# Kernel optimization log

Hardware: AMD Instinct MI355X
Metric: run time of the kernel (lower is better)

## Reference

```python
import jax, jax.numpy as jnp
import numpy as np

B, N, C = 8, 1374, 768
H = 12
HD = C // H  # 64
HIDDEN = int(C * 4.0)  # 3072
EPS = 1e-5


def setup_inputs() -> dict:
    key = jax.random.key(0)
    ks = jax.random.split(key, 12)
    s = 0.02
    return {
        "x": jax.random.normal(ks[0], (B, N, C), jnp.float32),
        "rope_freqs": jax.random.normal(ks[1], (1, N, 1, HD), jnp.float32),
        "ln1_g": jnp.ones((C,), jnp.float32),
        "ln1_b": jnp.zeros((C,), jnp.float32),
        "qkv_w": jax.random.normal(ks[2], (3 * C, C), jnp.float32) * s,
        "qkv_b": jnp.zeros((3 * C,), jnp.float32),
        "proj_w": jax.random.normal(ks[3], (C, C), jnp.float32) * s,
        "proj_b": jnp.zeros((C,), jnp.float32),
        "ln2_g": jnp.ones((C,), jnp.float32),
        "ln2_b": jnp.zeros((C,), jnp.float32),
        "w1": jax.random.normal(ks[4], (HIDDEN, C), jnp.float32) * s,
        "b1": jnp.zeros((HIDDEN,), jnp.float32),
        "w2": jax.random.normal(ks[5], (HIDDEN, C), jnp.float32) * s,
        "b2": jnp.zeros((HIDDEN,), jnp.float32),
        "w3": jax.random.normal(ks[6], (C, HIDDEN), jnp.float32) * s,
        "b3": jnp.zeros((C,), jnp.float32),
    }


def _layernorm(x, g, b):
    mu = jnp.mean(x, axis=-1, keepdims=True)
    var = jnp.mean(jnp.square(x - mu), axis=-1, keepdims=True)
    return (x - mu) * jax.lax.rsqrt(var + EPS) * g + b


def _rotate_half(x):
    x1, x2 = jnp.split(x, 2, axis=-1)
    return jnp.concatenate([-x2, x1], axis=-1)


def _apply_rope(q, k, freqs):
    # freqs: [1, N, 1, HD] -> [1, 1, N, HD] (matches torch permute(0,2,1,3))
    f = jnp.transpose(freqs, (0, 2, 1, 3))
    cos, sin = jnp.cos(f), jnp.sin(f)
    q_rot = q * cos + _rotate_half(q) * sin
    k_rot = k * cos + _rotate_half(k) * sin
    return q_rot, k_rot


def reference(x, rope_freqs, ln1_g, ln1_b, qkv_w, qkv_b, proj_w, proj_b,
              ln2_g, ln2_b, w1, b1, w2, b2, w3, b3):
    scale = HD ** -0.5
    # --- Attention branch ---
    h = _layernorm(x, ln1_g, ln1_b)
    qkv = jnp.einsum('bnc,dc->bnd', h, qkv_w) + qkv_b          # [B,N,3C]
    qkv = qkv.reshape(B, N, 3, H, HD).transpose(2, 0, 3, 1, 4)  # [3,B,H,N,HD]
    q, k, v = qkv[0], qkv[1], qkv[2]
    # rope_freqs covers all N tokens -> n_special = 0 path
    q, k = _apply_rope(q, k, rope_freqs)
    attn = jnp.einsum('bhnd,bhmd->bhnm', q, k) * scale          # [B,H,N,N]
    attn = jax.nn.softmax(attn, axis=-1)
    o = jnp.einsum('bhnm,bhmd->bhnd', attn, v)                  # [B,H,N,HD]
    o = o.transpose(0, 2, 1, 3).reshape(B, N, C)
    o = jnp.einsum('bnc,dc->bnd', o, proj_w) + proj_b
    x = x + o
    # --- SwiGLU MLP branch ---
    h2 = _layernorm(x, ln2_g, ln2_b)
    x1 = jnp.einsum('bnc,hc->bnh', h2, w1) + b1
    x2 = jnp.einsum('bnc,hc->bnh', h2, w2) + b2
    hid = jax.nn.silu(x1) * x2
    mlp_out = jnp.einsum('bnh,ch->bnc', hid, w3) + b3
    return x + mlp_out
```

## Files before the change

### kernel.cpp

```cpp
#include <hip/hip_runtime.h>
#include <stdint.h>

#define B_ 8
#define N_ 1374
#define C_ 768
#define H_ 12
#define HD_ 64
#define HID_ 3072
#define M_ (B_*N_)
#define MPAD_ 11008
#define QT_ 22
#define QT2_ 11

typedef __attribute__((ext_vector_type(8))) short short8;
typedef __attribute__((ext_vector_type(4))) float f32x4;
typedef __attribute__((ext_vector_type(4))) _Float16 half4;
typedef __attribute__((ext_vector_type(2))) _Float16 half2v;

__device__ __forceinline__ unsigned short f2bf(float f) {
  unsigned u = __float_as_uint(f);
  u += 0x7FFF + ((u >> 16) & 1);
  return (unsigned short)(u >> 16);
}
__device__ __forceinline__ float bf2f(unsigned short h) {
  return __uint_as_float(((unsigned)h) << 16);
}

__device__ __forceinline__ half2v pkrtz(float a, float b) {
  return __builtin_bit_cast(half2v, __builtin_amdgcn_cvt_pkrtz(a, b));
}

#if __has_builtin(__builtin_amdgcn_global_load_lds)
#define HAVE_GLL 1
#endif

__device__ __forceinline__ void gld16(const unsigned short* g, unsigned short* l) {
#ifdef HAVE_GLL
  __builtin_amdgcn_global_load_lds((const __attribute__((address_space(1))) void*)g,
                                   (__attribute__((address_space(3))) void*)l, 16, 0, 0);
#else
  *(short8*)l = *(const short8*)g;
#endif
}

__global__ __launch_bounds__(256) void cvt5_kernel(
    const float* __restrict__ s0, const float* __restrict__ s1,
    const float* __restrict__ s2, const float* __restrict__ s3,
    const float* __restrict__ s4, unsigned short* __restrict__ out) {
  int id = blockIdx.x * 256 + threadIdx.x;
  const float* src; int off;
  if (id < 442368)        { src = s0; off = id; }
  else if (id < 589824)   { src = s1; off = id - 442368; }
  else if (id < 1179648)  { src = s2; off = id - 589824; }
  else if (id < 1769472)  { src = s3; off = id - 1179648; }
  else                    { src = s4; off = id - 1769472; }
  float4 v = ((const float4*)src)[off];
  ushort4 o;
  o.x = f2bf(v.x); o.y = f2bf(v.y); o.z = f2bf(v.z); o.w = f2bf(v.w);
  ((ushort4*)out)[id] = o;
}

__global__ __launch_bounds__(256) void ln_kernel(const float* __restrict__ in,
    const float* __restrict__ g, const float* __restrict__ bta,
    unsigned short* __restrict__ out) {
  int row = blockIdx.x;
  int t = threadIdx.x;
  const float* xr = in + (size_t)row * C_;
  float v0 = xr[t], v1 = xr[t + 256], v2 = xr[t + 512];
  float s1 = v0 + v1 + v2;
  float s2 = v0*v0 + v1*v1 + v2*v2;
  for (int off = 1; off < 64; off <<= 1) {
    s1 += __shfl_xor(s1, off, 64);
    s2 += __shfl_xor(s2, off, 64);
  }
  __shared__ float r1[4], r2[4];
  int wave = t >> 6, lane = t & 63;
  if (lane == 0) { r1[wave] = s1; r2[wave] = s2; }
  __syncthreads();
  float tot1 = r1[0] + r1[1] + r1[2] + r1[3];
  float tot2 = r2[0] + r2[1] + r2[2] + r2[3];
  float mu = tot1 * (1.0f / C_);
  float var = tot2 * (1.0f / C_) - mu * mu;
  float rs = rsqrtf(var + 1e-5f);
  size_t ob = (size_t)row * C_;
  out[ob + t]       = f2bf((v0 - mu) * rs * g[t]       + bta[t]);
  out[ob + t + 256] = f2bf((v1 - mu) * rs * g[t + 256] + bta[t + 256]);
  out[ob + t + 512] = f2bf((v2 - mu) * rs * g[t + 512] + bta[t + 512]);
}

template<int EPI, int ROPE, int TM, int SWZ>
__global__ __launch_bounds__(256, (TM == 64) ? 4 : 2) void gemm_bt(
    const unsigned short* __restrict__ A,
    const unsigned short* __restrict__ W,
    void* __restrict__ outp,
    const float* __restrict__ bias0,
    const float* __restrict__ resid,
    const float* __restrict__ freqs,
    int K, int ldo, int Mvalid, int X)
{
  constexpr int MI = TM / 32;
  __shared__ __align__(16) unsigned short As[2][TM * 32];
  __shared__ __align__(16) unsigned short Bs[2][4096];
  const int t = threadIdx.x;
  const int lane = t & 63;
  const int wave = t >> 6;
  const int wm = (wave >> 1) * (TM / 2);
  const int wn = (wave & 1) * 64;
  const int lr = lane & 15;
  const int lg = lane >> 4;
  const int lk = lg * 8;
  int bx, by;
  if (SWZ) {
    int Y = gridDim.x / X;
    int lin = blockIdx.x;
    int sgsz = X * 8;
    int sg = lin / sgsz;
    int base_y = sg * 8;
    int rows = Y - base_y; if (rows > 8) rows = 8;
    int within = lin - sg * sgsz;
    by = base_y + within % rows;
    bx = within / rows;
  } else {
    bx = blockIdx.x % X;
    by = blockIdx.x / X;
  }
  const int tm0 = by * TM;
  const int tn0 = bx * 128;
  const int r0 = t >> 2;
  const int c0 = (t & 3) * 8;
  const unsigned short* ga0 = A + (size_t)(tm0 + r0) * K + c0;
  const unsigned short* ga1 = A + (size_t)(tm0 + 64 + r0) * K + c0;
  const unsigned short* gb0 = W + (size_t)(tn0 + r0) * K + c0;
  const unsigned short* gb1 = W + (size_t)(tn0 + 64 + r0) * K + c0;
  f32x4 zero = {0.f, 0.f, 0.f, 0.f};
  f32x4 acc[MI][4];
#pragma unroll
  for (int mi = 0; mi < MI; ++mi)
#pragma unroll
    for (int ni = 0; ni < 4; ++ni) acc[mi][ni] = zero;

  for (int kt = 0; kt < K; kt += 64) {
    __syncthreads();
    gld16(ga0 + kt,      &As[0][t * 8]);
    gld16(ga0 + kt + 32, &As[1][t * 8]);
    if (TM == 128) {
      gld16(ga1 + kt,      &As[0][2048 + t * 8]);
      gld16(ga1 + kt + 32, &As[1][2048 + t * 8]);
    }
    gld16(gb0 + kt,      &Bs[0][t * 8]);
    gld16(gb1 + kt,      &Bs[0][2048 + t * 8]);
    gld16(gb0 + kt + 32, &Bs[1][t * 8]);
    gld16(gb1 + kt + 32, &Bs[1][2048 + t * 8]);
    __syncthreads();
#pragma unroll
    for (int u = 0; u < 2; ++u) {
      short8 af[MI], bfr[4];
#pragma unroll
      for (int mi = 0; mi < MI; ++mi) af[mi] = *(const short8*)&As[u][(wm + mi * 16 + lr) * 32 + lk];
#pragma unroll
      for (int ni = 0; ni < 4; ++ni) bfr[ni] = *(const short8*)&Bs[u][(wn + ni * 16 + lr) * 32 + lk];
#pragma unroll
      for (int mi = 0; mi < MI; ++mi)
#pragma unroll
        for (int ni = 0; ni < 4; ++ni)
          acc[mi][ni] = __builtin_amdgcn_mfma_f32_16x16x32_bf16(af[mi], bfr[ni], acc[mi][ni], 0, 0, 0);
    }
  }

  if (EPI == 0) {
    bool dorope = ROPE && ((tn0 + wn) < 1536);
#pragma unroll
    for (int mi = 0; mi < MI; ++mi) {
#pragma unroll
      for (int p = 0; p < 2; ++p) {
        int col1 = tn0 + wn + p * 16 + lr;
        int col2 = col1 + 32;
        float bv1 = bias0[col1], bv2 = bias0[col2];
        int e = p * 16 + lr;
#pragma unroll
        for (int r = 0; r < 4; ++r) {
          int row = tm0 + wm + mi * 16 + lg * 4 + r;
          float v1 = acc[mi][p][r] + bv1;
          float v2 = acc[mi][p + 2][r] + bv2;
          float o1 = v1, o2 = v2;
          if (dorope) {
            int n = row % N_;
            float f1 = freqs[n * HD_ + e];
            float f2 = freqs[n * HD_ + e + 32];
            float c1, s1, c2, s2;
            __sincosf(f1, &s1, &c1);
            __sincosf(f2, &s2, &c2);
            o1 = v1 * c1 - v2 * s1;
            o2 = v2 * c2 + v1 * s2;
          }
          size_t base = (size_t)row * ldo;
          ((unsigned short*)outp)[base + col1] = f2bf(o1);
          ((unsigned short*)outp)[base + col2] = f2bf(o2);
        }
      }
    }
  } else {
#pragma unroll
    for (int mi = 0; mi < MI; ++mi) {
#pragma unroll
      for (int ni = 0; ni < 4; ++ni) {
        int col = tn0 + wn + ni * 16 + lr;
        float bval = bias0[col];
#pragma unroll
        for (int r = 0; r < 4; ++r) {
          int row = tm0 + wm + mi * 16 + lg * 4 + r;
          float v = acc[mi][ni][r] + bval;
          size_t idx = (size_t)row * ldo + col;
          if (EPI == 1) {
            if (row < Mvalid) ((float*)outp)[idx] = resid[idx] + v;
          } else {
            if (row < Mvalid) ((float*)outp)[idx] = ((float*)outp)[idx] + v;
          }
        }
      }
    }
  }
}

__global__ __launch_bounds__(256, 2) void gemm_w12_swiglu(
    const unsigned short* __restrict__ A,
    const unsigned short* __restrict__ W1,
    const unsigned short* __restrict__ W2,
    unsigned short* __restrict__ hid,
    const float* __restrict__ b1,
    const float* __restrict__ b2)
{
  __shared__ __align__(16) unsigned short As[2][4096];
  __shared__ __align__(16) unsigned short B1s[2][2048];
  __shared__ __align__(16) unsigned short B2s[2][2048];
  const int t = threadIdx.x;
  const int lane = t & 63;
  const int wave = t >> 6;
  const int wm = (wave >> 1) * 64;
  const int wn = (wave & 1) * 32;
  const int lr = lane & 15;
  const int lg = lane >> 4;
  const int lk = lg * 8;
  const int tm0 = blockIdx.y * 128;
  const int tn0 = blockIdx.x * 64;
  const int r0 = t >> 2;
  const int c0 = (t & 3) * 8;
  const unsigned short* ga0 = A + (size_t)(tm0 + r0) * 768 + c0;
  const unsigned short* ga1 = A + (size_t)(tm0 + 64 + r0) * 768 + c0;
  const unsigned short* g1 = W1 + (size_t)(tn0 + r0) * 768 + c0;
  const unsigned short* g2 = W2 + (size_t)(tn0 + r0) * 768 + c0;
  f32x4 zero = {0.f, 0.f, 0.f, 0.f};
  f32x4 acc1[4][2], acc2[4][2];
#pragma unroll
  for (int mi = 0; mi < 4; ++mi)
#pragma unroll
    for (int ni = 0; ni < 2; ++ni) { acc1[mi][ni] = zero; acc2[mi][ni] = zero; }

  for (int kt = 0; kt < 768; kt += 64) {
    __syncthreads();
    gld16(ga0 + kt,      &As[0][t * 8]);
    gld16(ga1 + kt,      &As[0][2048 + t * 8]);
    gld16(ga0 + kt + 32, &As[1][t * 8]);
    gld16(ga1 + kt + 32, &As[1][2048 + t * 8]);
    gld16(g1 + kt,       &B1s[0][t * 8]);
    gld16(g1 + kt + 32,  &B1s[1][t * 8]);
    gld16(g2 + kt,       &B2s[0][t * 8]);
    gld16(g2 + kt + 32,  &B2s[1][t * 8]);
    __syncthreads();
#pragma unroll
    for (int u = 0; u < 2; ++u) {
      short8 af[4], b1f[2], b2f[2];
#pragma unroll
      for (int mi = 0; mi < 4; ++mi) af[mi] = *(const short8*)&As[u][(wm + mi * 16 + lr) * 32 + lk];
#pragma unroll
      for (int ni = 0; ni < 2; ++ni) {
        b1f[ni] = *(const short8*)&B1s[u][(wn + ni * 16 + lr) * 32 + lk];
        b2f[ni] = *(const short8*)&B2s[u][(wn + ni * 16 + lr) * 32 + lk];
      }
#pragma unroll
      for (int mi = 0; mi < 4; ++mi)
#pragma unroll
        for (int ni = 0; ni < 2; ++ni) {
          acc1[mi][ni] = __builtin_amdgcn_mfma_f32_16x16x32_bf16(af[mi], b1f[ni], acc1[mi][ni], 0, 0, 0);
          acc2[mi][ni] = __builtin_amdgcn_mfma_f32_16x16x32_bf16(af[mi], b2f[ni], acc2[mi][ni], 0, 0, 0);
        }
    }
  }
#pragma unroll
  for (int mi = 0; mi < 4; ++mi) {
#pragma unroll
    for (int ni = 0; ni < 2; ++ni) {
      int col = tn0 + wn + ni * 16 + lr;
      float bv1 = b1[col], bv2 = b2[col];
#pragma unroll
      for (int r = 0; r < 4; ++r) {
        int row = tm0 + wm + mi * 16 + lg * 4 + r;
        float a1 = acc1[mi][ni][r] + bv1;
        float a2 = acc2[mi][ni][r] + bv2;
        float h = a1 / (1.f + __expf(-a1)) * a2;
        hid[(size_t)row * HID_ + col] = f2bf(h);
      }
    }
  }
}

struct FalseT { static constexpr bool value = false; };
struct TrueT  { static constexpr bool value = true;  };

__global__ __launch_bounds__(256, 2) void attn_kernel(
    const unsigned short* __restrict__ qkv,
    unsigned short* __restrict__ o2)
{
  __shared__ __align__(16) unsigned short Ks[2][64 * 80];
  __shared__ __align__(16) _Float16 Vt[2][64 * 72];
  int bidx = blockIdx.x;
  int qt = bidx % QT2_;
  int bh = bidx / QT2_;
  int head = bh % H_;
  int b = bh / H_;
  int t = threadIdx.x, lane = t & 63, wave = t >> 6;
  int lr = lane & 15, lg = lane >> 4;

  short8 bq[2][2];
#pragma unroll
  for (int s = 0; s < 2; ++s) {
    int m = qt * 128 + wave * 32 + s * 16 + lr;
    int mc = (m < N_) ? m : (N_ - 1);
    const unsigned short* qrow = qkv + (size_t)(b * N_ + mc) * 2304 + head * HD_;
    bq[s][0] = *(const short8*)(qrow + lg * 8);
    bq[s][1] = *(const short8*)(qrow + 32 + lg * 8);
  }

  f32x4 zero = {0.f, 0.f, 0.f, 0.f};
  f32x4 acc[2][4];
#pragma unroll
  for (int s = 0; s < 2; ++s)
#pragma unroll
    for (int dt = 0; dt < 4; ++dt) acc[s][dt] = zero;
  float den[2] = {0.f, 0.f};

  const int kr0 = t >> 3;
  const int kc  = (t & 7) * 8;
  const int vp  = t & 31;
  const int vc  = t >> 5;
  const unsigned short* kbase = qkv + (size_t)(b * N_) * 2304 + 768  + head * HD_ + kc;
  const unsigned short* vbase = qkv + (size_t)(b * N_) * 2304 + 1536 + head * HD_ + vc * 8;

  short8 krg[2], vrg[2];
  auto issue = [&](int jt) {
    int j0 = jt * 64 + kr0;        if (j0 >= N_) j0 = N_ - 1;
    int j1 = jt * 64 + kr0 + 32;   if (j1 >= N_) j1 = N_ - 1;
    int vj0 = jt * 64 + 2 * vp;    if (vj0 >= N_) vj0 = N_ - 1;
    int vj1 = jt * 64 + 2 * vp + 1; if (vj1 >= N_) vj1 = N_ - 1;
    krg[0] = *(const short8*)(kbase + (size_t)j0 * 2304);
    krg[1] = *(const short8*)(kbase + (size_t)j1 * 2304);
    vrg[0] = *(const short8*)(vbase + (size_t)vj0 * 2304);
    vrg[1] = *(const short8*)(vbase + (size_t)vj1 * 2304);
  };

  auto compute = [&](int jt, const unsigned short* ksb, const _Float16* vtb, auto tailc) {
    constexpr bool TAIL = decltype(tailc)::value;
#pragma unroll
    for (int st = 0; st < 4; ++st) {
      short8 ak0 = *(const short8*)&ksb[(st * 16 + lr) * 80 + lg * 8];
      short8 ak1 = *(const short8*)&ksb[(st * 16 + lr) * 80 + 32 + lg * 8];
      int jb = jt * 64 + st * 16 + lg * 4;
      half4 pf[2];
#pragma unroll
      for (int s = 0; s < 2; ++s) {
        f32x4 sc = zero;
        sc = __builtin_amdgcn_mfma_f32_16x16x32_bf16(ak0, bq[s][0], sc, 0, 0, 0);
        sc = __builtin_amdgcn_mfma_f32_16x16x32_bf16(ak1, bq[s][1], sc, 0, 0, 0);
        float p[4];
#pragma unroll
        for (int r = 0; r < 4; ++r) {
          float pv = exp2f(sc[r] * 0.18033688011112f);
          if (TAIL) pv = (jb + r < N_) ? pv : 0.f;
          p[r] = pv;
        }
        den[s] += (p[0] + p[1]) + (p[2] + p[3]);
        union { half4 v; half2v h[2]; } pu;
        pu.h[0] = pkrtz(p[0], p[1]);
        pu.h[1] = pkrtz(p[2], p[3]);
        pf[s] = pu.v;
      }
#pragma unroll
      for (int dt = 0; dt < 4; ++dt) {
        half4 bv = *(const half4*)&vtb[(dt * 16 + lr) * 72 + st * 16 + lg * 4];
        acc[0][dt] = __builtin_amdgcn_mfma_f32_16x16x16f16(pf[0], bv, acc[0][dt], 0, 0, 0);
        acc[1][dt] = __builtin_amdgcn_mfma_f32_16x16x16f16(pf[1], bv, acc[1][dt], 0, 0, 0);
      }
    }
  };

  issue(0);
  int cur = 0;
  for (int jt = 0; jt < QT_; ++jt) {
    unsigned short* ksb = &Ks[cur][0];
    _Float16* vtb = &Vt[cur][0];
    *(short8*)&ksb[kr0 * 80 + kc] = krg[0];
    *(short8*)&ksb[(kr0 + 32) * 80 + kc] = krg[1];
#pragma unroll
    for (int i = 0; i < 8; ++i) {
      float lo = bf2f((unsigned short)vrg[0][i]);
      float hi = bf2f((unsigned short)vrg[1][i]);
      half2v w = pkrtz(lo, hi);
      *(half2v*)&vtb[(vc * 8 + i) * 72 + 2 * vp] = w;
    }
    __syncthreads();
    issue(jt + 1);
    if (jt == QT_ - 1) compute(jt, ksb, vtb, TrueT{});
    else               compute(jt, ksb, vtb, FalseT{});
    cur ^= 1;
  }

#pragma unroll
  for (int s = 0; s < 2; ++s) {
    den[s] += __shfl_xor(den[s], 16, 64);
    den[s] += __shfl_xor(den[s], 32, 64);
  }
#pragma unroll
  for (int s = 0; s < 2; ++s) {
#pragma unroll
    for (int r = 0; r < 4; ++r) {
      float dm = __shfl(den[s], lg * 4 + r, 64);
      int m = qt * 128 + wave * 32 + s * 16 + lg * 4 + r;
      if (m < N_) {
        float invd = 1.f / dm;
        unsigned short* orow = o2 + (size_t)(b * N_ + m) * C_ + head * HD_;
#pragma unroll
        for (int dt = 0; dt < 4; ++dt)
          orow[dt * 16 + lr] = f2bf(acc[s][dt][r] * invd);
      }
    }
  }
}

extern "C" void kernel_launch(void* const* d_in, const int* in_sizes, int n_in,
                              void* d_out, int out_size, void* d_ws, size_t ws_size,
                              hipStream_t stream) {
  const float* x      = (const float*)d_in[0];
  const float* freqs  = (const float*)d_in[1];
  const float* ln1_g  = (const float*)d_in[2];
  const float* ln1_b  = (const float*)d_in[3];
  const float* qkv_w  = (const float*)d_in[4];
  const float* qkv_b  = (const float*)d_in[5];
  const float* proj_w = (const float*)d_in[6];
  const float* proj_b = (const float*)d_in[7];
  const float* ln2_g  = (const float*)d_in[8];
  const float* ln2_b  = (const float*)d_in[9];
  const float* w1     = (const float*)d_in[10];
  const float* b1     = (const float*)d_in[11];
  const float* w2     = (const float*)d_in[12];
  const float* b2     = (const float*)d_in[13];
  const float* w3     = (const float*)d_in[14];
  const float* b3     = (const float*)d_in[15];
  float* out = (float*)d_out;
  char* ws = (char*)d_ws;

  unsigned short* hB     = (unsigned short*)(ws + 0);
  unsigned short* wqkvB  = (unsigned short*)(ws + 16908288);
  unsigned short* wprojB = (unsigned short*)(ws + 20447232);
  unsigned short* w12B   = (unsigned short*)(ws + 21626880);
  unsigned short* w3B    = (unsigned short*)(ws + 31064064);
  unsigned short* qkvB   = (unsigned short*)(ws + 35782656);
  unsigned short* o2B    = (unsigned short*)(ws + 86507520);
  unsigned short* hidB   = qkvB;

  cvt5_kernel<<<9216, 256, 0, stream>>>(qkv_w, proj_w, w1, w2, w3, wqkvB);

  ln_kernel<<<M_, 256, 0, stream>>>(x, ln1_g, ln1_b, hB);
  gemm_bt<0, 1, 128, 1><<<18 * 86, 256, 0, stream>>>(hB, wqkvB, qkvB, qkv_b, nullptr, freqs, 768, 2304, M_, 18);
  attn_kernel<<<B_ * H_ * QT2_, 256, 0, stream>>>(qkvB, o2B);
  gemm_bt<1, 0, 64, 1><<<6 * 172, 256, 0, stream>>>(o2B, wprojB, out, proj_b, x, nullptr, 768, 768, M_, 6);

  ln_kernel<<<M_, 256, 0, stream>>>(out, ln2_g, ln2_b, hB);
  gemm_w12_swiglu<<<dim3(48, 86), 256, 0, stream>>>(hB, w12B, w12B + 3072 * 768, hidB, b1, b2);
  gemm_bt<3, 0, 64, 1><<<6 * 172, 256, 0, stream>>>(hidB, w3B, out, b3, nullptr, nullptr, 3072, 768, M_, 6);
}
```

Before: 551.9 us.

## Fold softmax scale into Q, store V as fp16, compute denominators via MFMA

The QKV GEMM epilogue now pre-multiplies Q by the softmax scale (in log2 units) and writes V directly as fp16 instead of bf16. That lets the attention kernel skip the per-element scale multiply and the bf16-to-fp16 conversion of V tiles. The softmax denominator is now accumulated with an extra MFMA against a ones vector, replacing the per-thread adds and cross-lane shuffles. Launch bounds are raised to target 4 blocks per SM, which may force register spilling.

```diff
diff --git a/kernel.cpp b/kernel.cpp
--- a/kernel.cpp
+++ b/kernel.cpp
@@ -12,6 +12,8 @@
 #define QT_ 22
 #define QT2_ 11
 
+#define QSC_ 0.18033688011112042f
+
 typedef __attribute__((ext_vector_type(8))) short short8;
 typedef __attribute__((ext_vector_type(4))) float f32x4;
 typedef __attribute__((ext_vector_type(4))) _Float16 half4;
@@ -24,6 +26,9 @@
 }
 __device__ __forceinline__ float bf2f(unsigned short h) {
   return __uint_as_float(((unsigned)h) << 16);
+}
+__device__ __forceinline__ unsigned short f2h(float f) {
+  return __builtin_bit_cast(unsigned short, (_Float16)f);
 }
 
 __device__ __forceinline__ half2v pkrtz(float a, float b) {
@@ -169,6 +174,8 @@
 
   if (EPI == 0) {
     bool dorope = ROPE && ((tn0 + wn) < 1536);
+    bool isq    = ROPE && ((tn0 + wn) < 768);
+    bool isv    = ROPE && ((tn0 + wn) >= 1536);
 #pragma unroll
     for (int mi = 0; mi < MI; ++mi) {
 #pragma unroll
@@ -193,9 +200,15 @@
             o1 = v1 * c1 - v2 * s1;
             o2 = v2 * c2 + v1 * s2;
           }
+          if (isq) { o1 *= QSC_; o2 *= QSC_; }
           size_t base = (size_t)row * ldo;
-          ((unsigned short*)outp)[base + col1] = f2bf(o1);
-          ((unsigned short*)outp)[base + col2] = f2bf(o2);
+          if (isv) {
+            ((unsigned short*)outp)[base + col1] = f2h(o1);
+            ((unsigned short*)outp)[base + col2] = f2h(o2);
+          } else {
+            ((unsigned short*)outp)[base + col1] = f2bf(o1);
+            ((unsigned short*)outp)[base + col2] = f2bf(o2);
+          }
         }
       }
     }
@@ -307,7 +320,7 @@
 struct FalseT { static constexpr bool value = false; };
 struct TrueT  { static constexpr bool value = true;  };
 
-__global__ __launch_bounds__(256, 2) void attn_kernel(
+__global__ __launch_bounds__(256, 4) void attn_kernel(
     const unsigned short* __restrict__ qkv,
     unsigned short* __restrict__ o2)
 {
@@ -333,11 +346,13 @@
 
   f32x4 zero = {0.f, 0.f, 0.f, 0.f};
   f32x4 acc[2][4];
-#pragma unroll
-  for (int s = 0; s < 2; ++s)
+  f32x4 dacc[2];
+#pragma unroll
+  for (int s = 0; s < 2; ++s) {
+    dacc[s] = zero;
 #pragma unroll
     for (int dt = 0; dt < 4; ++dt) acc[s][dt] = zero;
-  float den[2] = {0.f, 0.f};
+  }
 
   const int kr0 = t >> 3;
   const int kc  = (t & 7) * 8;
@@ -358,6 +373,8 @@
     vrg[1] = *(const short8*)(vbase + (size_t)vj1 * 2304);
   };
 
+  const half4 vones = {(_Float16)1.f, (_Float16)1.f, (_Float16)1.f, (_Float16)1.f};
+
   auto compute = [&](int jt, const unsigned short* ksb, const _Float16* vtb, auto tailc) {
     constexpr bool TAIL = decltype(tailc)::value;
 #pragma unroll
@@ -374,16 +391,17 @@
         float p[4];
 #pragma unroll
         for (int r = 0; r < 4; ++r) {
-          float pv = exp2f(sc[r] * 0.18033688011112f);
+          float pv = exp2f(sc[r]);
           if (TAIL) pv = (jb + r < N_) ? pv : 0.f;
           p[r] = pv;
         }
-        den[s] += (p[0] + p[1]) + (p[2] + p[3]);
         union { half4 v; half2v h[2]; } pu;
         pu.h[0] = pkrtz(p[0], p[1]);
         pu.h[1] = pkrtz(p[2], p[3]);
         pf[s] = pu.v;
       }
+      dacc[0] = __builtin_amdgcn_mfma_f32_16x16x16f16(pf[0], vones, dacc[0], 0, 0, 0);
+      dacc[1] = __builtin_amdgcn_mfma_f32_16x16x16f16(pf[1], vones, dacc[1], 0, 0, 0);
 #pragma unroll
       for (int dt = 0; dt < 4; ++dt) {
         half4 bv = *(const half4*)&vtb[(dt * 16 + lr) * 72 + st * 16 + lg * 4];
@@ -402,10 +420,9 @@
     *(short8*)&ksb[(kr0 + 32) * 80 + kc] = krg[1];
 #pragma unroll
     for (int i = 0; i < 8; ++i) {
-      float lo = bf2f((unsigned short)vrg[0][i]);
-      float hi = bf2f((unsigned short)vrg[1][i]);
-      half2v w = pkrtz(lo, hi);
-      *(half2v*)&vtb[(vc * 8 + i) * 72 + 2 * vp] = w;
+      unsigned lo = (unsigned short)vrg[0][i];
+      unsigned hi = (unsigned short)vrg[1][i];
+      *(unsigned*)&Vt[cur][(vc * 8 + i) * 72 + 2 * vp] = lo | (hi << 16);
     }
     __syncthreads();
     issue(jt + 1);
@@ -416,14 +433,9 @@
 
 #pragma unroll
   for (int s = 0; s < 2; ++s) {
-    den[s] += __shfl_xor(den[s], 16, 64);
-    den[s] += __shfl_xor(den[s], 32, 64);
-  }
-#pragma unroll
-  for (int s = 0; s < 2; ++s) {
 #pragma unroll
     for (int r = 0; r < 4; ++r) {
-      float dm = __shfl(den[s], lg * 4 + r, 64);
+      float dm = dacc[s][r];
       int m = qt * 128 + wave * 32 + s * 16 + lg * 4 + r;
       if (m < N_) {
         float invd = 1.f / dm;
```

New measurement: 531.6 us. -3.7%, faster.
